# Optimization experiments

Measured on AMD Instinct MI355X. Metric: run time of the kernel, lower is better.

## Reference

```python
import jax, jax.numpy as jnp
import numpy as np

SIGMA = 2.0
EPS = 1e-8

N, P = 4, 64
Z, Y, X = 32, 128, 128


def setup_inputs() -> dict:
    key = jax.random.key(0)
    k1, k2 = jax.random.split(key)
    logits = jax.random.normal(k1, (N, 1, Z, Y, X), dtype=jnp.float32)
    # float (z,y,x) coordinates uniformly inside the grid
    dims = jnp.array([Z, Y, X], dtype=jnp.float32)
    pts = jax.random.uniform(k2, (N, P, 3), dtype=jnp.float32) * dims
    return {"logits": logits, "pts": pts}


def reference(logits, pts):
    # logits: [N,1,Z,Y,X]; pts: [N,P,3] in (z,y,x)
    n, _, z, y, x = logits.shape
    dt = logits.dtype
    s = jax.nn.sigmoid(logits[:, 0])  # [N,Z,Y,X]

    zz = jnp.arange(z, dtype=dt)
    yy = jnp.arange(y, dtype=dt)
    xx = jnp.arange(x, dtype=dt)

    # squared distances, broadcast to [N,P,Z,Y,X] only at the sum
    dz2 = (zz[None, None, :, None, None] - pts[:, :, 0, None, None, None]) ** 2  # [N,P,Z,1,1]
    dy2 = (yy[None, None, None, :, None] - pts[:, :, 1, None, None, None]) ** 2  # [N,P,1,Y,1]
    dx2 = (xx[None, None, None, None, :] - pts[:, :, 2, None, None, None]) ** 2  # [N,P,1,1,X]

    K = jnp.exp(-(dz2 + dy2 + dx2) / (2.0 * SIGMA * SIGMA))  # [N,P,Z,Y,X]
    denom = K.sum(axis=1)  # [N,Z,Y,X]  (alpha_bg == 0)
    w = s / jnp.maximum(denom, EPS)  # [N,Z,Y,X]
    # m_p = sum_v K[p,v] * s[v] / denom[v]
    m = jnp.einsum('npzyx,nzyx->np', K, w)  # [N,P]
    point_term = -jnp.log(jnp.maximum(m, EPS)).mean(axis=1)  # [N]
    return point_term.mean()  # reduction='mean'
```

## Files before the change

### kernel.cpp

```cpp
#include <hip/hip_runtime.h>
#include <math.h>

constexpr int N_ = 4, P_ = 64, Z_ = 32, Y_ = 128, X_ = 128;
constexpr float EPSF = 1e-8f;
constexpr float INV2S2 = 0.125f;

__global__ __launch_bounds__(256, 2) void k_fused(const float* __restrict__ logits,
                                                  const float* __restrict__ pts,
                                                  float* __restrict__ part) {
    const int b = blockIdx.x;
    const int n  = b >> 7;
    const int z  = (b >> 2) & 31;
    const int y0 = ((b >> 1) & 1) * 64;
    const int x0 = (b & 1) * 64;

    const int tid = threadIdx.x;
    const int lane = tid & 63;
    const int wid = tid >> 6;

    __shared__ float ptsn[192];
    __shared__ float kzy[64 * 64];
    __shared__ float wsum[4][64];

    if (tid < 192) ptsn[tid] = pts[n * 192 + tid];
    __syncthreads();

    for (int i = tid; i < 64 * 64; i += 256) {
        int row = i >> 6, p = i & 63;
        float dz = (float)z - ptsn[p * 3 + 0];
        float dy = (float)(y0 + row) - ptsn[p * 3 + 1];
        kzy[i] = __expf(-(dz * dz + dy * dy) * INV2S2);
    }

    const int x = x0 + lane;
    float kxr[64], macc[64];
    #pragma unroll
    for (int p = 0; p < 64; ++p) {
        float dx = (float)x - ptsn[p * 3 + 2];
        kxr[p] = __expf(-dx * dx * INV2S2);
        macc[p] = 0.0f;
    }
    __syncthreads();

    const float* lbase = logits + (size_t)((n * Z_ + z) * Y_ + y0) * X_ + x;

    float lg = lbase[wid * X_];
    #pragma unroll 1
    for (int pass = 0; pass < 16; ++pass) {
        const int row = pass * 4 + wid;
        float lg_next = 0.0f;
        if (pass < 15) lg_next = lbase[(row + 4) * X_];

        const float4* kr = (const float4*)(&kzy[row * 64]);
        float kkx[64];
        float d0 = 0.f, d1 = 0.f, d2 = 0.f, d3 = 0.f;
        #pragma unroll
        for (int q = 0; q < 16; ++q) {
            const float4 k4 = kr[q];
            kkx[4*q+0] = k4.x * kxr[4*q+0]; d0 += kkx[4*q+0];
            kkx[4*q+1] = k4.y * kxr[4*q+1]; d1 += kkx[4*q+1];
            kkx[4*q+2] = k4.z * kxr[4*q+2]; d2 += kkx[4*q+2];
            kkx[4*q+3] = k4.w * kxr[4*q+3]; d3 += kkx[4*q+3];
        }
        const float denom = (d0 + d1) + (d2 + d3);
        const float w = 1.0f / ((1.0f + __expf(-lg)) * fmaxf(denom, EPSF));

        #pragma unroll
        for (int p = 0; p < 64; ++p) macc[p] = fmaf(kkx[p], w, macc[p]);
        lg = lg_next;
    }

    float* v = macc;
#define RED_STAGE(D)                                              \
    {                                                             \
        const bool hi = (lane & (D)) != 0;                        \
        _Pragma("unroll")                                         \
        for (int i = 0; i < (D); ++i) {                           \
            float mine = hi ? v[i + (D)] : v[i];                  \
            float send = hi ? v[i] : v[i + (D)];                  \
            float got = __shfl_xor(send, (D), 64);                \
            v[i] = mine + got;                                    \
        }                                                         \
    }
    RED_STAGE(32) RED_STAGE(16) RED_STAGE(8)
    RED_STAGE(4)  RED_STAGE(2)  RED_STAGE(1)
#undef RED_STAGE
    wsum[wid][lane] = v[0];
    __syncthreads();
    if (tid < 64) {
        float s = (wsum[0][tid] + wsum[1][tid]) + (wsum[2][tid] + wsum[3][tid]);
        part[b * 64 + tid] = s;
    }
}

__global__ __launch_bounds__(1024) void k_finish(const float* __restrict__ part,
                                                 float* __restrict__ out) {
    const int t = threadIdx.x;
    const int pair = t & 255;
    const int quarter = t >> 8;
    const int n = pair >> 6, p = pair & 63;

    const float* base = part + (size_t)(n * 128 + quarter * 32) * 64 + p;
    float s0 = 0.f, s1 = 0.f, s2 = 0.f, s3 = 0.f;
    #pragma unroll 2
    for (int j = 0; j < 32; j += 4) {
        s0 += base[(j + 0) * 64];
        s1 += base[(j + 1) * 64];
        s2 += base[(j + 2) * 64];
        s3 += base[(j + 3) * 64];
    }
    __shared__ float red[4][256];
    red[quarter][pair] = (s0 + s1) + (s2 + s3);
    __syncthreads();

    if (t < 256) {
        const float m = (red[0][t] + red[1][t]) + (red[2][t] + red[3][t]);
        float l = -logf(fmaxf(m, EPSF));
        #pragma unroll
        for (int off = 32; off > 0; off >>= 1) l += __shfl_xor(l, off, 64);
        __shared__ float red2[4];
        if ((t & 63) == 0) red2[t >> 6] = l;
        __syncthreads();
        if (t == 0) out[0] = (red2[0] + red2[1] + red2[2] + red2[3]) * (1.0f / 256.0f);
    }
}

extern "C" void kernel_launch(void* const* d_in, const int* in_sizes, int n_in,
                              void* d_out, int out_size, void* d_ws, size_t ws_size,
                              hipStream_t stream) {
    const float* logits = (const float*)d_in[0];
    const float* pts    = (const float*)d_in[1];
    float* part = (float*)d_ws;
    float* out  = (float*)d_out;

    k_fused<<<dim3(512), dim3(256), 0, stream>>>(logits, pts, part);
    k_finish<<<dim3(1), dim3(1024), 0, stream>>>(part, out);
}
```

Before: 74.93 us.

## Process two x-columns per thread to halve y-row kernel loads and shuffle reductions

Each block now covers 32 y-rows by the full 128 x-width, and each thread handles x=lane and x=lane+64 with two separable x-kernel register arrays. The y/z kernel row read from shared memory is reused for both columns, and the p-accumulation factors k_zy out, so per-pass work is about 4 FMAs per p for two voxels. Because each block's x-range doubles, the number of partial vectors fed to the cross-lane shuffle reduction per voxel halves. The cost is higher register pressure (three 64-float arrays) and shared memory rows being loaded twice per pass.

```diff
diff --git a/kernel.cpp b/kernel.cpp
--- a/kernel.cpp
+++ b/kernel.cpp
@@ -11,63 +11,76 @@
     const int b = blockIdx.x;
     const int n  = b >> 7;
     const int z  = (b >> 2) & 31;
-    const int y0 = ((b >> 1) & 1) * 64;
-    const int x0 = (b & 1) * 64;
+    const int y0 = (b & 3) * 32;
 
     const int tid = threadIdx.x;
     const int lane = tid & 63;
     const int wid = tid >> 6;
 
     __shared__ float ptsn[192];
-    __shared__ float kzy[64 * 64];
+    __shared__ float kzy[32 * 64];
     __shared__ float wsum[4][64];
 
     if (tid < 192) ptsn[tid] = pts[n * 192 + tid];
     __syncthreads();
 
-    for (int i = tid; i < 64 * 64; i += 256) {
+    for (int i = tid; i < 32 * 64; i += 256) {
         int row = i >> 6, p = i & 63;
         float dz = (float)z - ptsn[p * 3 + 0];
         float dy = (float)(y0 + row) - ptsn[p * 3 + 1];
         kzy[i] = __expf(-(dz * dz + dy * dy) * INV2S2);
     }
 
-    const int x = x0 + lane;
-    float kxr[64], macc[64];
+    float kxA[64], kxB[64], macc[64];
     #pragma unroll
     for (int p = 0; p < 64; ++p) {
-        float dx = (float)x - ptsn[p * 3 + 2];
-        kxr[p] = __expf(-dx * dx * INV2S2);
+        float pxv = ptsn[p * 3 + 2];
+        float dxA = (float)lane - pxv;
+        float dxB = (float)(lane + 64) - pxv;
+        kxA[p] = __expf(-dxA * dxA * INV2S2);
+        kxB[p] = __expf(-dxB * dxB * INV2S2);
         macc[p] = 0.0f;
     }
     __syncthreads();
 
-    const float* lbase = logits + (size_t)((n * Z_ + z) * Y_ + y0) * X_ + x;
+    const float* lbase = logits + (size_t)((n * Z_ + z) * Y_ + y0) * X_ + lane;
 
-    float lg = lbase[wid * X_];
+    float lgA = lbase[wid * X_];
+    float lgB = lbase[wid * X_ + 64];
     #pragma unroll 1
-    for (int pass = 0; pass < 16; ++pass) {
+    for (int pass = 0; pass < 8; ++pass) {
         const int row = pass * 4 + wid;
-        float lg_next = 0.0f;
-        if (pass < 15) lg_next = lbase[(row + 4) * X_];
+        float lgA_n = 0.0f, lgB_n = 0.0f;
+        if (pass < 7) {
+            lgA_n = lbase[(row + 4) * X_];
+            lgB_n = lbase[(row + 4) * X_ + 64];
+        }
 
         const float4* kr = (const float4*)(&kzy[row * 64]);
-        float kkx[64];
-        float d0 = 0.f, d1 = 0.f, d2 = 0.f, d3 = 0.f;
+        float a0 = 0.f, a1 = 0.f, a2 = 0.f, a3 = 0.f;
+        float b0 = 0.f, b1 = 0.f, b2 = 0.f, b3 = 0.f;
         #pragma unroll
         for (int q = 0; q < 16; ++q) {
             const float4 k4 = kr[q];
-            kkx[4*q+0] = k4.x * kxr[4*q+0]; d0 += kkx[4*q+0];
-            kkx[4*q+1] = k4.y * kxr[4*q+1]; d1 += kkx[4*q+1];
-            kkx[4*q+2] = k4.z * kxr[4*q+2]; d2 += kkx[4*q+2];
-            kkx[4*q+3] = k4.w * kxr[4*q+3]; d3 += kkx[4*q+3];
+            a0 = fmaf(k4.x, kxA[4*q+0], a0); b0 = fmaf(k4.x, kxB[4*q+0], b0);
+            a1 = fmaf(k4.y, kxA[4*q+1], a1); b1 = fmaf(k4.y, kxB[4*q+1], b1);
+            a2 = fmaf(k4.z, kxA[4*q+2], a2); b2 = fmaf(k4.z, kxB[4*q+2], b2);
+            a3 = fmaf(k4.w, kxA[4*q+3], a3); b3 = fmaf(k4.w, kxB[4*q+3], b3);
         }
-        const float denom = (d0 + d1) + (d2 + d3);
-        const float w = 1.0f / ((1.0f + __expf(-lg)) * fmaxf(denom, EPSF));
+        const float dA = (a0 + a1) + (a2 + a3);
+        const float dB = (b0 + b1) + (b2 + b3);
+        const float wA = 1.0f / ((1.0f + __expf(-lgA)) * fmaxf(dA, EPSF));
+        const float wB = 1.0f / ((1.0f + __expf(-lgB)) * fmaxf(dB, EPSF));
 
         #pragma unroll
-        for (int p = 0; p < 64; ++p) macc[p] = fmaf(kkx[p], w, macc[p]);
-        lg = lg_next;
+        for (int q = 0; q < 16; ++q) {
+            const float4 k4 = kr[q];
+            macc[4*q+0] = fmaf(k4.x, fmaf(kxB[4*q+0], wB, kxA[4*q+0] * wA), macc[4*q+0]);
+            macc[4*q+1] = fmaf(k4.y, fmaf(kxB[4*q+1], wB, kxA[4*q+1] * wA), macc[4*q+1]);
+            macc[4*q+2] = fmaf(k4.z, fmaf(kxB[4*q+2], wB, kxA[4*q+2] * wA), macc[4*q+2]);
+            macc[4*q+3] = fmaf(k4.w, fmaf(kxB[4*q+3], wB, kxA[4*q+3] * wA), macc[4*q+3]);
+        }
+        lgA = lgA_n; lgB = lgB_n;
     }
 
     float* v = macc;
```

Result: slower. 76.71 us (+2.4%).

## Recast separable Gaussian sums as bf16 MFMA matmuls per z-slab

Applied to the files above, without the earlier changes.

Replaces the per-thread scalar FMA loops with two bf16 MFMA GEMMs. The first computes denom as Kzy times Kx^T for a 64x128 y-x tile. The second contracts the weight tile with Kx to get per-point partial sums, which are then scaled by Kzy and reduced with shuffles. Swizzled LDS layouts are used for the bf16 operands, and blocks now cover a full x row, so the grid shrinks from 512 to 256 blocks. The change trades fp32 accuracy for bf16 in the kernels, the denominators and the weights, and cuts the number of blocks, which lowers parallelism.

```diff
diff --git a/kernel.cpp b/kernel.cpp
--- a/kernel.cpp
+++ b/kernel.cpp
@@ -5,92 +5,148 @@
 constexpr float EPSF = 1e-8f;
 constexpr float INV2S2 = 0.125f;
 
-__global__ __launch_bounds__(256, 2) void k_fused(const float* __restrict__ logits,
-                                                  const float* __restrict__ pts,
-                                                  float* __restrict__ part) {
+typedef short v8s __attribute__((ext_vector_type(8)));
+typedef float v4f __attribute__((ext_vector_type(4)));
+
+__device__ __forceinline__ short bf16(float f) {
+    unsigned u = __float_as_uint(f);
+    u = u + 0x7fffu + ((u >> 16) & 1u);
+    return (short)(u >> 16);
+}
+
+__global__ __launch_bounds__(256) void k_main(const float* __restrict__ logits,
+                                              const float* __restrict__ pts,
+                                              float* __restrict__ part) {
     const int b = blockIdx.x;
-    const int n  = b >> 7;
-    const int z  = (b >> 2) & 31;
-    const int y0 = ((b >> 1) & 1) * 64;
-    const int x0 = (b & 1) * 64;
+    const int n  = b >> 6;
+    const int z  = (b >> 1) & 31;
+    const int y0 = (b & 1) * 64;
 
-    const int tid = threadIdx.x;
+    const int tid  = threadIdx.x;
     const int lane = tid & 63;
-    const int wid = tid >> 6;
+    const int w    = tid >> 6;
+    const int m    = lane & 15;
+    const int quad = lane >> 4;
 
     __shared__ float ptsn[192];
-    __shared__ float kzy[64 * 64];
-    __shared__ float wsum[4][64];
+    __shared__ short kxTB[128 * 64];
+    __shared__ short WB[64 * 128];
+    __shared__ float psum[64];
 
     if (tid < 192) ptsn[tid] = pts[n * 192 + tid];
     __syncthreads();
 
-    for (int i = tid; i < 64 * 64; i += 256) {
-        int row = i >> 6, p = i & 63;
-        float dz = (float)z - ptsn[p * 3 + 0];
-        float dy = (float)(y0 + row) - ptsn[p * 3 + 1];
-        kzy[i] = __expf(-(dz * dz + dy * dy) * INV2S2);
+    for (int i = tid; i < 128 * 64; i += 256) {
+        int x = i >> 6, p = i & 63;
+        float dx = (float)x - ptsn[p * 3 + 2];
+        float e = __expf(-dx * dx * INV2S2);
+        kxTB[x * 64 + (((p >> 3) ^ (x & 7)) * 8) + (p & 7)] = bf16(e);
     }
 
-    const int x = x0 + lane;
-    float kxr[64], macc[64];
-    #pragma unroll
-    for (int p = 0; p < 64; ++p) {
-        float dx = (float)x - ptsn[p * 3 + 2];
-        kxr[p] = __expf(-dx * dx * INV2S2);
-        macc[p] = 0.0f;
+    v8s a1[2];
+    {
+        float yv = (float)(y0 + w * 16 + m);
+        #pragma unroll
+        for (int ks = 0; ks < 2; ++ks) {
+            #pragma unroll
+            for (int j = 0; j < 8; ++j) {
+                int p = ks * 32 + quad * 8 + j;
+                float dz = (float)z - ptsn[p * 3 + 0];
+                float dy = yv - ptsn[p * 3 + 1];
+                a1[ks][j] = bf16(__expf(-(dz * dz + dy * dy) * INV2S2));
+            }
+        }
     }
     __syncthreads();
 
-    const float* lbase = logits + (size_t)((n * Z_ + z) * Y_ + y0) * X_ + x;
-
-    float lg = lbase[wid * X_];
-    #pragma unroll 1
-    for (int pass = 0; pass < 16; ++pass) {
-        const int row = pass * 4 + wid;
-        float lg_next = 0.0f;
-        if (pass < 15) lg_next = lbase[(row + 4) * X_];
-
-        const float4* kr = (const float4*)(&kzy[row * 64]);
-        float kkx[64];
-        float d0 = 0.f, d1 = 0.f, d2 = 0.f, d3 = 0.f;
+    v4f acc1[8];
+    #pragma unroll
+    for (int nt = 0; nt < 8; ++nt) acc1[nt] = (v4f)(0.f);
+    #pragma unroll
+    for (int ks = 0; ks < 2; ++ks) {
         #pragma unroll
-        for (int q = 0; q < 16; ++q) {
-            const float4 k4 = kr[q];
-            kkx[4*q+0] = k4.x * kxr[4*q+0]; d0 += kkx[4*q+0];
-            kkx[4*q+1] = k4.y * kxr[4*q+1]; d1 += kkx[4*q+1];
-            kkx[4*q+2] = k4.z * kxr[4*q+2]; d2 += kkx[4*q+2];
-            kkx[4*q+3] = k4.w * kxr[4*q+3]; d3 += kkx[4*q+3];
+        for (int nt = 0; nt < 8; ++nt) {
+            int row = nt * 16 + m;
+            int c = ks * 4 + quad;
+            v8s bf = *(const v8s*)&kxTB[row * 64 + ((c ^ (row & 7)) * 8)];
+            acc1[nt] = __builtin_amdgcn_mfma_f32_16x16x32_bf16(a1[ks], bf, acc1[nt], 0, 0, 0);
         }
-        const float denom = (d0 + d1) + (d2 + d3);
-        const float w = 1.0f / ((1.0f + __expf(-lg)) * fmaxf(denom, EPSF));
-
-        #pragma unroll
-        for (int p = 0; p < 64; ++p) macc[p] = fmaf(kkx[p], w, macc[p]);
-        lg = lg_next;
     }
 
-    float* v = macc;
-#define RED_STAGE(D)                                              \
-    {                                                             \
-        const bool hi = (lane & (D)) != 0;                        \
-        _Pragma("unroll")                                         \
-        for (int i = 0; i < (D); ++i) {                           \
-            float mine = hi ? v[i + (D)] : v[i];                  \
-            float send = hi ? v[i] : v[i + (D)];                  \
-            float got = __shfl_xor(send, (D), 64);                \
-            v[i] = mine + got;                                    \
-        }                                                         \
+    {
+        const float* lb = logits + (size_t)((n * Z_ + z) * Y_ + y0) * X_;
+        float lgs[8][4];
+        #pragma unroll
+        for (int nt = 0; nt < 8; ++nt)
+            #pragma unroll
+            for (int reg = 0; reg < 4; ++reg)
+                lgs[nt][reg] = lb[(w * 16 + quad * 4 + reg) * 128 + nt * 16 + m];
+        #pragma unroll
+        for (int nt = 0; nt < 8; ++nt) {
+            #pragma unroll
+            for (int reg = 0; reg < 4; ++reg) {
+                int yl = w * 16 + quad * 4 + reg;
+                int x  = nt * 16 + m;
+                float wv = 1.0f / ((1.0f + __expf(-lgs[nt][reg])) *
+                                   fmaxf(acc1[nt][reg], EPSF));
+                WB[yl * 128 + (((x >> 3) ^ (yl & 15)) * 8) + (x & 7)] = bf16(wv);
+            }
+        }
     }
-    RED_STAGE(32) RED_STAGE(16) RED_STAGE(8)
-    RED_STAGE(4)  RED_STAGE(2)  RED_STAGE(1)
-#undef RED_STAGE
-    wsum[wid][lane] = v[0];
+
+    v8s a2[4];
+    {
+        float px = ptsn[(w * 16 + m) * 3 + 2];
+        #pragma unroll
+        for (int ks = 0; ks < 4; ++ks) {
+            #pragma unroll
+            for (int j = 0; j < 8; ++j) {
+                float dx = (float)(ks * 32 + quad * 8 + j) - px;
+                a2[ks][j] = bf16(__expf(-dx * dx * INV2S2));
+            }
+        }
+    }
     __syncthreads();
-    if (tid < 64) {
-        float s = (wsum[0][tid] + wsum[1][tid]) + (wsum[2][tid] + wsum[3][tid]);
-        part[b * 64 + tid] = s;
+
+    v4f acc2[4];
+    #pragma unroll
+    for (int nt = 0; nt < 4; ++nt) acc2[nt] = (v4f)(0.f);
+    #pragma unroll
+    for (int ks = 0; ks < 4; ++ks) {
+        #pragma unroll
+        for (int nt = 0; nt < 4; ++nt) {
+            int row = nt * 16 + m;
+            int c = ks * 4 + quad;
+            v8s bf = *(const v8s*)&WB[row * 128 + ((c ^ (row & 15)) * 8)];
+            acc2[nt] = __builtin_amdgcn_mfma_f32_16x16x32_bf16(a2[ks], bf, acc2[nt], 0, 0, 0);
+        }
     }
+
+    float s[4] = {0.f, 0.f, 0.f, 0.f};
+    #pragma unroll
+    for (int reg = 0; reg < 4; ++reg) {
+        int p = w * 16 + quad * 4 + reg;
+        float pz = ptsn[p * 3 + 0], py = ptsn[p * 3 + 1];
+        float dz = (float)z - pz;
+        #pragma unroll
+        for (int nt = 0; nt < 4; ++nt) {
+            float dy = (float)(y0 + nt * 16 + m) - py;
+            float kzy = __expf(-(dz * dz + dy * dy) * INV2S2);
+            s[reg] = fmaf(acc2[nt][reg], kzy, s[reg]);
+        }
+    }
+    #pragma unroll
+    for (int reg = 0; reg < 4; ++reg)
+        #pragma unroll
+        for (int off = 1; off < 16; off <<= 1)
+            s[reg] += __shfl_xor(s[reg], off, 64);
+    if (m == 0) {
+        #pragma unroll
+        for (int reg = 0; reg < 4; ++reg)
+            psum[w * 16 + quad * 4 + reg] = s[reg];
+    }
+    __syncthreads();
+    if (tid < 64) part[b * 64 + tid] = psum[tid];
 }
 
 __global__ __launch_bounds__(1024) void k_finish(const float* __restrict__ part,
@@ -100,10 +156,10 @@
     const int quarter = t >> 8;
     const int n = pair >> 6, p = pair & 63;
 
-    const float* base = part + (size_t)(n * 128 + quarter * 32) * 64 + p;
+    const float* base = part + (size_t)(n * 64 + quarter * 16) * 64 + p;
     float s0 = 0.f, s1 = 0.f, s2 = 0.f, s3 = 0.f;
-    #pragma unroll 2
-    for (int j = 0; j < 32; j += 4) {
+    #pragma unroll
+    for (int j = 0; j < 16; j += 4) {
         s0 += base[(j + 0) * 64];
         s1 += base[(j + 1) * 64];
         s2 += base[(j + 2) * 64];
@@ -114,8 +170,8 @@
     __syncthreads();
 
     if (t < 256) {
-        const float m = (red[0][t] + red[1][t]) + (red[2][t] + red[3][t]);
-        float l = -logf(fmaxf(m, EPSF));
+        const float mv = (red[0][t] + red[1][t]) + (red[2][t] + red[3][t]);
+        float l = -logf(fmaxf(mv, EPSF));
         #pragma unroll
         for (int off = 32; off > 0; off >>= 1) l += __shfl_xor(l, off, 64);
         __shared__ float red2[4];
@@ -133,6 +189,6 @@
     float* part = (float*)d_ws;
     float* out  = (float*)d_out;
 
-    k_fused<<<dim3(512), dim3(256), 0, stream>>>(logits, pts, part);
+    k_main<<<dim3(256), dim3(256), 0, stream>>>(logits, pts, part);
     k_finish<<<dim3(1), dim3(1024), 0, stream>>>(part, out);
 }
```

New measurement: 66.03 us. -11.9%, faster.
